# Performance work log

Hardware: AMD Instinct MI355X
Metric: run time of the kernel (lower is better)

Reference implementation:

```python
import jax, jax.numpy as jnp
import numpy as np

N = 100_000        # event nodes
E = 1_600_000      # directed edges (avg degree 16)
DIM = 256          # coordinate box size (input_dimension)
POOL = 4           # pool_size of all pooling layers


def gconv(nodes, feats, edges, W):
    """PointNet-style graph conv: msg = [f_src ; pos_src - pos_dst] @ W, max-aggregated at dst."""
    src, dst = edges[0], edges[1]
    msg = jnp.concatenate([feats[src], nodes[src] - nodes[dst]], axis=1) @ W  # [E, out]
    agg = jax.ops.segment_max(msg, dst, num_segments=nodes.shape[0])
    return jnp.where(jnp.isfinite(agg), agg, 0.0)  # nodes with no in-edges -> 0


def pool(nodes, feats, edges, pool_size, grid, self_loop):
    """Voxel-grid max pooling: cluster nodes into grid^3 cells, max-pool features,
    remap edges to cluster ids (duplicate edges are harmless under max aggregation)."""
    cell = jnp.clip(jnp.floor(nodes / pool_size).astype(jnp.int32), 0, grid - 1)
    cid = (cell[:, 0] * grid + cell[:, 1]) * grid + cell[:, 2]
    n_cells = grid ** 3
    nf = jax.ops.segment_max(feats, cid, num_segments=n_cells)
    nf = jnp.where(jnp.isfinite(nf), nf, 0.0)  # empty cells -> 0
    ii = jnp.arange(n_cells)
    nn = jnp.stack([ii // (grid * grid), (ii // grid) % grid, ii % grid], axis=1).astype(feats.dtype)
    ne = cid[edges]
    if self_loop:
        loops = jnp.tile(jnp.arange(n_cells, dtype=ne.dtype), (2, 1))
        ne = jnp.concatenate([ne, loops], axis=1)
    return nn, nf, ne


def forward(nodes, features, edges, W1, W2, W3, W4, W5, W6, W7, Wl, bl):
    relu = lambda x: jnp.maximum(x, 0.0)
    x = relu(gconv(nodes, features, edges, W1))              # [N, 8]
    x = relu(gconv(nodes, x, edges, W2))                     # [N, 16]
    nodes, x, edges = pool(nodes, x, edges, POOL, DIM // POOL, True)   # 64^3 cells
    x = relu(gconv(nodes, x, edges, W3))                     # [64^3, 32]
    x = relu(gconv(nodes, x, edges, W4))                     # [64^3, 32]
    nodes, x, edges = pool(nodes, x, edges, POOL, 64 // POOL, False)   # 16^3 cells
    x = relu(gconv(nodes, x, edges, W5))                     # [16^3, 64]
    x = relu(gconv(nodes, x, edges, W6))
    x = relu(gconv(nodes, x, edges, W7))
    # QuantGraphPoolOut: max-pool onto fixed 4x4x4 grid, flatten to [1, 4096]
    cell = jnp.clip(jnp.floor(nodes / POOL).astype(jnp.int32), 0, 3)
    cid = (cell[:, 0] * 4 + cell[:, 1]) * 4 + cell[:, 2]
    xo = jax.ops.segment_max(x, cid, num_segments=64)        # [64, 64]
    xo = jnp.where(jnp.isfinite(xo), xo, 0.0).reshape(1, -1)  # [1, 4096]
    # dropout is identity in eval mode
    return xo @ Wl + bl                                      # [1, 100]


def setup_inputs() -> dict:
    key = jax.random.key(0)
    ks = jax.random.split(key, 12)

    def w(k, i, o):  # conv weight: (input_dim + 3 pos dims, output_dim)
        return jax.random.normal(k, (i + 3, o), dtype=jnp.float32) * (1.0 / np.sqrt(i + 3))

    nodes = jax.random.uniform(ks[0], (N, 3), dtype=jnp.float32) * DIM
    features = jax.random.normal(ks[1], (N, 1), dtype=jnp.float32)
    edges = jax.random.randint(ks[2], (2, E), 0, N, dtype=jnp.int32)
    return {
        "nodes": nodes, "features": features, "edges": edges,
        "W1": w(ks[3], 1, 8), "W2": w(ks[4], 8, 16), "W3": w(ks[5], 16, 32),
        "W4": w(ks[6], 32, 32), "W5": w(ks[7], 32, 64), "W6": w(ks[8], 64, 64),
        "W7": w(ks[9], 64, 64),
        "Wl": jax.random.normal(ks[10], (4096, 100), dtype=jnp.float32) * (1.0 / 64.0),
        "bl": jnp.zeros((100,), dtype=jnp.float32),
    }


def reference(nodes, features, edges, W1, W2, W3, W4, W5, W6, W7, Wl, bl):
    return forward(nodes, features, edges, W1, W2, W3, W4, W5, W6, W7, Wl, bl)
```

## Files before the change

kernel.cpp:

```cpp
#include <hip/hip_runtime.h>

#define NN 100000
#define NE 1600000
#define C1 262144
#define C2 4096
#define BSH 7
#define BSZ 128
#define NB 782
#define PA_EDGES 8192
#define PA_IT (PA_EDGES / 256)
#define JMASK 0xFFFFF

__device__ __forceinline__ int parent2(int c) {
    return ((c >> 14) << 8) | (((c >> 8) & 15) << 4) | ((c >> 2) & 15);
}
__device__ __forceinline__ float4 max4(float4 a, float4 b) {
    return make_float4(fmaxf(a.x, b.x), fmaxf(a.y, b.y), fmaxf(a.z, b.z), fmaxf(a.w, b.w));
}
__device__ __forceinline__ float4 fma4(float s, float4 w, float4 acc) {
    return make_float4(s * w.x + acc.x, s * w.y + acc.y, s * w.z + acc.z, s * w.w + acc.w);
}

__global__ __launch_bounds__(256)
void cidhist_k(const float* __restrict__ nodes, int* __restrict__ cid,
               int* __restrict__ cntN) {
    int i = blockIdx.x * 256 + threadIdx.x;
    if (i >= NN) return;
    int cx = min(max((int)floorf(nodes[3 * i]     * 0.25f), 0), 63);
    int cy = min(max((int)floorf(nodes[3 * i + 1] * 0.25f), 0), 63);
    int cz = min(max((int)floorf(nodes[3 * i + 2] * 0.25f), 0), 63);
    int c = (cx * 64 + cy) * 64 + cz;
    cid[i] = c;
    atomicAdd(&cntN[c], 1);
}

__global__ __launch_bounds__(256)
void oclist_k(const int* __restrict__ cntN, int* __restrict__ oclist,
              int* __restrict__ jmap, int* __restrict__ ocount) {
    int c = blockIdx.x * 256 + threadIdx.x;
    bool occ = cntN[c] > 0;
    unsigned long long b = __ballot(occ);
    int lane = threadIdx.x & 63;
    int cnt = __popcll(b);
    int base = 0;
    if (cnt) {
        if (lane == 0) base = atomicAdd(ocount, cnt);
        base = __shfl(base, 0);
    }
    int pre = __popcll(b & ((1ull << lane) - 1));
    int j = occ ? base + pre : -1;
    jmap[c] = j;
    if (occ) oclist[j] = c;
}

__global__ __launch_bounds__(256)
void scan1_k(const int* __restrict__ cnt, int n, int* __restrict__ offs,
             int* __restrict__ bsum) {
    __shared__ int ws[4];
    int t = threadIdx.x, lane = t & 63, w = t >> 6;
    int base = blockIdx.x * 2048 + t * 8;
    int v[8]; int s = 0;
    #pragma unroll
    for (int i = 0; i < 8; ++i) { v[i] = (base + i < n) ? cnt[base + i] : 0; s += v[i]; }
    int sc = s;
    #pragma unroll
    for (int off = 1; off < 64; off <<= 1) { int o = __shfl_up(sc, off); if (lane >= off) sc += o; }
    if (lane == 63) ws[w] = sc;
    __syncthreads();
    int wbase = 0;
    for (int i = 0; i < w; ++i) wbase += ws[i];
    int run = wbase + sc - s;
    #pragma unroll
    for (int i = 0; i < 8; ++i) { if (base + i < n) offs[base + i] = run; run += v[i]; }
    if (t == 255) bsum[blockIdx.x] = wbase + sc;
}

__global__ __launch_bounds__(256)
void scan2_k(int* __restrict__ bsum, int nb) {
    __shared__ int ws[4];
    int t = threadIdx.x, lane = t & 63, w = t >> 6;
    int v = (t < nb) ? bsum[t] : 0;
    int sc = v;
    #pragma unroll
    for (int off = 1; off < 64; off <<= 1) { int o = __shfl_up(sc, off); if (lane >= off) sc += o; }
    if (lane == 63) ws[w] = sc;
    __syncthreads();
    int wbase = 0;
    for (int i = 0; i < w; ++i) wbase += ws[i];
    if (t < nb) bsum[t] = wbase + sc - v;
    if (t == 255) bsum[nb] = ws[0] + ws[1] + ws[2] + ws[3];
}

__global__ __launch_bounds__(256)
void scan3_k(int* __restrict__ offs, int n, const int* __restrict__ bsum, int nb) {
    int i = blockIdx.x * 256 + threadIdx.x;
    if (i < n) offs[i] += bsum[i >> 11];
    else if (i == n) offs[n] = bsum[nb];
}

__global__ __launch_bounds__(256)
void nscatter_k(const int* __restrict__ cid, const int* __restrict__ offsN,
                int* __restrict__ cntN, int* __restrict__ rank, int* __restrict__ nidx) {
    int i = blockIdx.x * 256 + threadIdx.x;
    if (i >= NN) return;
    int c = cid[i];
    int pos = offsN[c] + atomicAdd(&cntN[c], -1) - 1;
    rank[i] = pos;
    nidx[pos] = i;
}

__global__ __launch_bounds__(256)
void permute_k(const int* __restrict__ nidx, const float* __restrict__ nodes,
               const float* __restrict__ feats, const int* __restrict__ cid,
               const int* __restrict__ jmap,
               float* __restrict__ pnodes, float* __restrict__ pfeat,
               int* __restrict__ jsrcP) {
    int d = blockIdx.x * 256 + threadIdx.x;
    if (d >= NN) return;
    int i = nidx[d];
    pnodes[3 * d]     = nodes[3 * i];
    pnodes[3 * d + 1] = nodes[3 * i + 1];
    pnodes[3 * d + 2] = nodes[3 * i + 2];
    pfeat[d] = feats[i];
    int c = cid[i];
    unsigned packed = (unsigned)jmap[c] | ((unsigned)parent2(c) << 20);
    jsrcP[d] = (int)packed;
}

__global__ __launch_bounds__(256)
void bhist_k(const int* __restrict__ edst, const int* __restrict__ rank,
             int* __restrict__ btot) {
    __shared__ int h[NB];
    int tid = threadIdx.x;
    for (int i = tid; i < NB; i += 256) h[i] = 0;
    __syncthreads();
    int base = blockIdx.x * PA_EDGES;
    for (int i = 0; i < PA_IT; ++i) {
        int e = base + i * 256 + tid;
        if (e < NE) atomicAdd(&h[rank[edst[e]] >> BSH], 1);
    }
    __syncthreads();
    for (int i = tid; i < NB; i += 256) if (h[i]) atomicAdd(&btot[i], h[i]);
}

__global__ __launch_bounds__(256)
void scanB_k(const int* __restrict__ btot, int* __restrict__ bbase,
             int* __restrict__ cursor) {
    __shared__ int ws[4];
    int t = threadIdx.x, lane = t & 63, w = t >> 6;
    int i0 = 4 * t;
    int v[4]; int s = 0;
    #pragma unroll
    for (int q = 0; q < 4; ++q) { v[q] = (i0 + q < NB) ? btot[i0 + q] : 0; s += v[q]; }
    int sc = s;
    #pragma unroll
    for (int off = 1; off < 64; off <<= 1) { int o = __shfl_up(sc, off); if (lane >= off) sc += o; }
    if (lane == 63) ws[w] = sc;
    __syncthreads();
    int wb = 0;
    for (int q = 0; q < w; ++q) wb += ws[q];
    int run = wb + sc - s;
    #pragma unroll
    for (int q = 0; q < 4; ++q) {
        if (i0 + q <= NB) { bbase[i0 + q] = run; if (i0 + q < NB) cursor[i0 + q] = run; }
        run += v[q];
    }
}

__global__ __launch_bounds__(256)
void passA_k(const int* __restrict__ esrc, const int* __restrict__ edst,
             const int* __restrict__ rank, int* __restrict__ cursor,
             int2* __restrict__ ebuf) {
    __shared__ int hist[NB];
    __shared__ int lofs[NB + 1];
    __shared__ int gbase[NB];
    __shared__ int cnt2[NB];
    __shared__ int2 stage[PA_EDGES];
    __shared__ unsigned short sbid[PA_EDGES];
    __shared__ int ws[4];
    int tid = threadIdx.x, lane = tid & 63, w = tid >> 6;
    for (int i = tid; i < NB; i += 256) { hist[i] = 0; cnt2[i] = 0; }
    __syncthreads();
    int base = blockIdx.x * PA_EDGES;
    for (int i = 0; i < PA_IT; ++i) {
        int e = base + i * 256 + tid;
        if (e < NE) atomicAdd(&hist[rank[edst[e]] >> BSH], 1);
    }
    __syncthreads();
    int i0 = 4 * tid;
    int v[4]; int s = 0;
    #pragma unroll
    for (int q = 0; q < 4; ++q) { v[q] = (i0 + q < NB) ? hist[i0 + q] : 0; s += v[q]; }
    int sc = s;
    #pragma unroll
    for (int off = 1; off < 64; off <<= 1) { int o = __shfl_up(sc, off); if (lane >= off) sc += o; }
    if (lane == 63) ws[w] = sc;
    __syncthreads();
    int wb = 0;
    for (int q = 0; q < w; ++q) wb += ws[q];
    int run = wb + sc - s;
    #pragma unroll
    for (int q = 0; q < 4; ++q) {
        if (i0 + q <= NB) lofs[i0 + q] = run;
        run += v[q];
    }
    __syncthreads();
    for (int b = tid; b < NB; b += 256) {
        int c = hist[b];
        gbase[b] = c ? atomicAdd(&cursor[b], c) : 0;
    }
    __syncthreads();
    for (int i = 0; i < PA_IT; ++i) {
        int e = base + i * 256 + tid;
        if (e < NE) {
            int rd = rank[edst[e]], rs = rank[esrc[e]];
            int b = rd >> BSH;
            int p = lofs[b] + atomicAdd(&cnt2[b], 1);
            stage[p] = make_int2(rs, rd);
            sbid[p] = (unsigned short)b;
        }
    }
    __syncthreads();
    int nval = min(PA_EDGES, NE - base);
    for (int k = tid; k < nval; k += 256) {
        int b = sbid[k];
        ebuf[gbase[b] + (k - lofs[b])] = stage[k];
    }
}

__global__ __launch_bounds__(256)
void passB_k(const int2* __restrict__ ebuf, const int* __restrict__ bbase,
             const int* __restrict__ jsrcP,
             int* __restrict__ offs0, int* __restrict__ srcs0, int* __restrict__ csrc0) {
    __shared__ int cnt[BSZ];
    __shared__ int pos[BSZ];
    __shared__ int ws[4];
    int b = blockIdx.x, tid = threadIdx.x, lane = tid & 63, w = tid >> 6;
    int d0 = b << BSH;
    int range = min(BSZ, NN - d0);
    if (tid < BSZ) cnt[tid] = 0;
    __syncthreads();
    int r0 = bbase[b], r1 = bbase[b + 1];
    for (int k = r0 + tid; k < r1; k += 256) atomicAdd(&cnt[ebuf[k].y & (BSZ - 1)], 1);
    __syncthreads();
    int v = (tid < BSZ) ? cnt[tid] : 0;
    int sc = v;
    #pragma unroll
    for (int off = 1; off < 64; off <<= 1) { int o = __shfl_up(sc, off); if (lane >= off) sc += o; }
    if (lane == 63) ws[w] = sc;
    __syncthreads();
    int wb = 0;
    for (int q = 0; q < w; ++q) wb += ws[q];
    int rel = wb + sc - v;
    if (tid < range) offs0[d0 + tid] = r0 + rel;
    if (tid == 0) offs0[min(d0 + BSZ, NN)] = r1;
    if (tid < BSZ) pos[tid] = r0 + rel;
    __syncthreads();
    for (int k = r0 + tid; k < r1; k += 256) {
        int2 pr = ebuf[k];
        int di = pr.y & (BSZ - 1);
        int p = atomicAdd(&pos[di], 1);
        int rs = pr.x;
        srcs0[p] = rs;
        csrc0[p] = jsrcP[rs];
    }
}

__global__ __launch_bounds__(256)
void masklist_k(const int* __restrict__ offsN, const int* __restrict__ offs0,
                const int* __restrict__ csrc0,
                int* __restrict__ l2off, int* __restrict__ l2num,
                int* __restrict__ l2src, int* __restrict__ l2cursor) {
    __shared__ unsigned long long words[64];
    __shared__ int wpre[64];
    __shared__ int sbase;
    int d2 = blockIdx.x, tid = threadIdx.x;
    if (tid < 64) words[tid] = 0;
    __syncthreads();
    int x2 = d2 >> 8, y2 = (d2 >> 4) & 15, z2 = d2 & 15;
    int child = tid >> 2, sub = tid & 3;
    int i = child >> 4, jj = (child >> 2) & 3, k = child & 3;
    int d1 = ((x2 * 4 + i) * 64 + (y2 * 4 + jj)) * 64 + (z2 * 4 + k);
    int e0 = offs0[offsN[d1]], e1 = offs0[offsN[d1 + 1]];
    for (int t = e0 + sub; t < e1; t += 4) {
        int s2 = (int)(((unsigned)csrc0[t]) >> 20);
        atomicOr(&words[s2 >> 6], 1ull << (s2 & 63));
    }
    __syncthreads();
    if (tid < 64) {
        int pc = __popcll(words[tid]);
        int sc = pc;
        #pragma unroll
        for (int off = 1; off < 64; off <<= 1) {
            int o = __shfl_up(sc, off);
            if (tid >= off) sc += o;
        }
        wpre[tid] = sc - pc;
        if (tid == 63) {
            l2num[d2] = sc;
            int bb = atomicAdd(l2cursor, sc);
            l2off[d2] = bb;
            sbase = bb;
        }
    }
    __syncthreads();
    if (tid < 64) {
        unsigned long long wb = words[tid];
        int p = sbase + wpre[tid];
        while (wb) {
            int b = __builtin_ctzll(wb);
            wb &= wb - 1;
            l2src[p++] = (tid << 6) | b;
        }
    }
}

template<int CI, int CO>
__global__ __launch_bounds__(256)
void xform0_k(const float* __restrict__ pnodes, const float* __restrict__ f,
              const float* __restrict__ W, float* __restrict__ h) {
    __shared__ float sW[(CI + 3) * CO];
    for (int i = threadIdx.x; i < (CI + 3) * CO; i += 256) sW[i] = W[i];
    __syncthreads();
    int gid = blockIdx.x * 256 + threadIdx.x;
    int i = gid / CO, ch = gid - i * CO;
    if (i >= NN) return;
    float s = pnodes[3 * i] * sW[CI * CO + ch] + pnodes[3 * i + 1] * sW[(CI + 1) * CO + ch]
            + pnodes[3 * i + 2] * sW[(CI + 2) * CO + ch];
    #pragma unroll
    for (int k = 0; k < CI; ++k) s += f[(size_t)i * CI + k] * sW[k * CO + ch];
    h[(size_t)i * CO + ch] = s;
}

__global__ __launch_bounds__(256)
void gatherL0f_k(const float* __restrict__ pnodes, const float* __restrict__ h1,
                 const float* __restrict__ W1pos,
                 const float* __restrict__ W2,
                 const int* __restrict__ offs, const int* __restrict__ srcs,
                 float* __restrict__ h2) {
    __shared__ float sW1[24];
    __shared__ float sW2[176];
    __shared__ float f1s[32][8];
    int tid = threadIdx.x;
    if (tid < 24) sW1[tid] = W1pos[tid];
    if (tid < 176) sW2[tid] = W2[tid];
    __syncthreads();
    int gid = blockIdx.x * 256 + tid;
    int d = gid >> 3, ch = gid & 7;
    int dbase = blockIdx.x * 32;
    if (d < NN) {
        float c = pnodes[3 * d] * sW1[ch] + pnodes[3 * d + 1] * sW1[8 + ch] + pnodes[3 * d + 2] * sW1[16 + ch];
        float m0 = c, m1 = c, m2 = c, m3 = c;
        int e0 = offs[d], e1 = offs[d + 1];
        int t = e0;
        for (; t + 4 <= e1; t += 4) {
            int s0 = srcs[t], s1 = srcs[t + 1], s2 = srcs[t + 2], s3 = srcs[t + 3];
            m0 = fmaxf(m0, h1[(size_t)s0 * 8 + ch]);
            m1 = fmaxf(m1, h1[(size_t)s1 * 8 + ch]);
            m2 = fmaxf(m2, h1[(size_t)s2 * 8 + ch]);
            m3 = fmaxf(m3, h1[(size_t)s3 * 8 + ch]);
        }
        for (; t < e1; ++t) m0 = fmaxf(m0, h1[(size_t)srcs[t] * 8 + ch]);
        f1s[d - dbase][ch] = fmaxf(fmaxf(m0, m1), fmaxf(m2, m3)) - c;
    }
    __syncthreads();
    #pragma unroll
    for (int rep = 0; rep < 2; ++rep) {
        int dL = (tid >> 4) + rep * 16, ch2 = tid & 15;
        int dg = dbase + dL;
        if (dg < NN) {
            float s = pnodes[3 * dg] * sW2[128 + ch2] + pnodes[3 * dg + 1] * sW2[144 + ch2]
                    + pnodes[3 * dg + 2] * sW2[160 + ch2];
            #pragma unroll
            for (int k = 0; k < 8; ++k) s += f1s[dL][k] * sW2[k * 16 + ch2];
            h2[(size_t)dg * 16 + ch2] = s;
        }
    }
}

__global__ __launch_bounds__(256)
void gatherL0v4_k(const float* __restrict__ pnodes, const float* __restrict__ h,
                  const float* __restrict__ Wpos,
                  const int* __restrict__ offs, const int* __restrict__ srcs,
                  float* __restrict__ out) {
    __shared__ float sW[48];
    int tid = threadIdx.x;
    if (tid < 48) sW[tid] = Wpos[tid];
    __syncthreads();
    int gid = blockIdx.x * 256 + tid;
    int d = gid >> 2, q = gid & 3;
    if (d >= NN) return;
    float px = pnodes[3 * d], py = pnodes[3 * d + 1], pz = pnodes[3 * d + 2];
    float4 w0 = *(const float4*)&sW[q * 4];
    float4 w1 = *(const float4*)&sW[16 + q * 4];
    float4 w2 = *(const float4*)&sW[32 + q * 4];
    float4 c = make_float4(px * w0.x + py * w1.x + pz * w2.x, px * w0.y + py * w1.y + pz * w2.y,
                           px * w0.z + py * w1.z + pz * w2.z, px * w0.w + py * w1.w + pz * w2.w);
    float4 m0 = c, m1 = c, m2 = c, m3 = c;
    int e0 = offs[d], e1 = offs[d + 1];
    int t = e0;
    for (; t + 4 <= e1; t += 4) {
        int s0 = srcs[t], s1 = srcs[t + 1], s2 = srcs[t + 2], s3 = srcs[t + 3];
        m0 = max4(m0, *(const float4*)&h[(size_t)s0 * 16 + q * 4]);
        m1 = max4(m1, *(const float4*)&h[(size_t)s1 * 16 + q * 4]);
        m2 = max4(m2, *(const float4*)&h[(size_t)s2 * 16 + q * 4]);
        m3 = max4(m3, *(const float4*)&h[(size_t)s3 * 16 + q * 4]);
    }
    for (; t < e1; ++t) m0 = max4(m0, *(const float4*)&h[(size_t)srcs[t] * 16 + q * 4]);
    float4 m = max4(max4(m0, m1), max4(m2, m3));
    *(float4*)&out[(size_t)d * 16 + q * 4] = make_float4(m.x - c.x, m.y - c.y, m.z - c.z, m.w - c.w);
}

__global__ __launch_bounds__(256)
void pxformL1_k(const float* __restrict__ f2, const int* __restrict__ offsN,
                const int* __restrict__ oclist, const int* __restrict__ ocount,
                const float* __restrict__ W3, float* __restrict__ h) {
    __shared__ float sW[19 * 32];
    __shared__ float nf[8][16];
    for (int i = threadIdx.x; i < 19 * 32; i += 256) sW[i] = W3[i];
    int gid = blockIdx.x * 256 + threadIdx.x;
    int j = gid >> 5, ch = gid & 31;
    int lj = threadIdx.x >> 5;
    bool valid = j < *ocount;
    int d = valid ? oclist[j] : 0;
    if (valid && ch < 16) {
        float m = 0.f;
        int n0 = offsN[d], n1 = offsN[d + 1];
        for (int n = n0; n < n1; ++n) m = fmaxf(m, f2[(size_t)n * 16 + ch]);
        nf[lj][ch] = m;
    }
    __syncthreads();
    if (!valid) return;
    float px = (float)(d >> 12), py = (float)((d >> 6) & 63), pz = (float)(d & 63);
    float s = px * sW[16 * 32 + ch] + py * sW[17 * 32 + ch] + pz * sW[18 * 32 + ch];
    #pragma unroll
    for (int k = 0; k < 16; ++k) s += nf[lj][k] * sW[k * 32 + ch];
    h[(size_t)j * 32 + ch] = s;
}

__global__ __launch_bounds__(256)
void gatherL1f_k(const float* __restrict__ h, const float* __restrict__ W3pos,
                 const float* __restrict__ W4,
                 const int* __restrict__ offsN, const int* __restrict__ offs0,
                 const int* __restrict__ csrc0,
                 const int* __restrict__ oclist, const int* __restrict__ ocount,
                 float* __restrict__ hnext) {
    __shared__ float sWp[96];
    __shared__ float sW4[35 * 32];
    __shared__ float gsT[32][33];
    int tid = threadIdx.x;
    if (tid < 96) sWp[tid] = W3pos[tid];
    for (int i = tid; i < 35 * 32; i += 256) sW4[i] = W4[i];
    __syncthreads();
    int gid = blockIdx.x * 256 + tid;
    int j = gid >> 3, q = gid & 7;
    int lj = tid >> 3;
    bool valid = j < *ocount;
    int d = 0;
    float px = 0, py = 0, pz = 0;
    float4 c = make_float4(0, 0, 0, 0);
    if (valid) {
        d = oclist[j];
        px = (float)(d >> 12); py = (float)((d >> 6) & 63); pz = (float)(d & 63);
        float4 w0 = *(const float4*)&sWp[q * 4];
        float4 w1 = *(const float4*)&sWp[32 + q * 4];
        float4 w2 = *(const float4*)&sWp[64 + q * 4];
        c = make_float4(px * w0.x + py * w1.x + pz * w2.x, px * w0.y + py * w1.y + pz * w2.y,
                        px * w0.z + py * w1.z + pz * w2.z, px * w0.w + py * w1.w + pz * w2.w);
        float4 self = *(const float4*)&h[(size_t)j * 32 + q * 4];
        float4 m0 = max4(c, self), m1 = m0, m2 = m0, m3 = m0;
        int e0 = offs0[offsN[d]], e1 = offs0[offsN[d + 1]];
        int t = e0;
        for (; t + 4 <= e1; t += 4) {
            int s0 = csrc0[t] & JMASK, s1 = csrc0[t + 1] & JMASK;
            int s2 = csrc0[t + 2] & JMASK, s3 = csrc0[t + 3] & JMASK;
            m0 = max4(m0, *(const float4*)&h[(size_t)s0 * 32 + q * 4]);
            m1 = max4(m1, *(const float4*)&h[(size_t)s1 * 32 + q * 4]);
            m2 = max4(m2, *(const float4*)&h[(size_t)s2 * 32 + q * 4]);
            m3 = max4(m3, *(const float4*)&h[(size_t)s3 * 32 + q * 4]);
        }
        for (; t < e1; ++t) m0 = max4(m0, *(const float4*)&h[(size_t)(csrc0[t] & JMASK) * 32 + q * 4]);
        float4 m = max4(max4(m0, m1), max4(m2, m3));
        gsT[q * 4 + 0][lj] = m.x - c.x;
        gsT[q * 4 + 1][lj] = m.y - c.y;
        gsT[q * 4 + 2][lj] = m.z - c.z;
        gsT[q * 4 + 3][lj] = m.w - c.w;
    }
    __syncthreads();
    if (!valid) return;
    float4 s4;
    {
        float4 w0 = *(const float4*)&sW4[32 * 32 + q * 4];
        float4 w1 = *(const float4*)&sW4[33 * 32 + q * 4];
        float4 w2 = *(const float4*)&sW4[34 * 32 + q * 4];
        s4 = make_float4(px * w0.x + py * w1.x + pz * w2.x, px * w0.y + py * w1.y + pz * w2.y,
                         px * w0.z + py * w1.z + pz * w2.z, px * w0.w + py * w1.w + pz * w2.w);
    }
    #pragma unroll
    for (int k = 0; k < 32; ++k) {
        float g = gsT[k][lj];
        s4 = fma4(g, *(const float4*)&sW4[k * 32 + q * 4], s4);
    }
    *(float4*)&hnext[(size_t)j * 32 + q * 4] = s4;
}

__global__ __launch_bounds__(256)
void gatherL1_k(const float* __restrict__ h, const float* __restrict__ Wpos,
                const int* __restrict__ offsN, const int* __restrict__ offs0,
                const int* __restrict__ csrc0,
                const int* __restrict__ oclist, const int* __restrict__ ocount,
                float* __restrict__ g) {
    __shared__ float sW[96];
    int tid = threadIdx.x;
    if (tid < 96) sW[tid] = Wpos[tid];
    __syncthreads();
    int gid = blockIdx.x * 256 + tid;
    int j = gid >> 3, q = gid & 7;
    if (j >= *ocount) return;
    int d = oclist[j];
    float px = (float)(d >> 12), py = (float)((d >> 6) & 63), pz = (float)(d & 63);
    float4 w0 = *(const float4*)&sW[q * 4];
    float4 w1 = *(const float4*)&sW[32 + q * 4];
    float4 w2 = *(const float4*)&sW[64 + q * 4];
    float4 c = make_float4(px * w0.x + py * w1.x + pz * w2.x, px * w0.y + py * w1.y + pz * w2.y,
                           px * w0.z + py * w1.z + pz * w2.z, px * w0.w + py * w1.w + pz * w2.w);
    float4 self = *(const float4*)&h[(size_t)j * 32 + q * 4];
    float4 m0 = max4(c, self), m1 = m0, m2 = m0, m3 = m0;
    int e0 = offs0[offsN[d]], e1 = offs0[offsN[d + 1]];
    int t = e0;
    for (; t + 4 <= e1; t += 4) {
        int s0 = csrc0[t] & JMASK, s1 = csrc0[t + 1] & JMASK;
        int s2 = csrc0[t + 2] & JMASK, s3 = csrc0[t + 3] & JMASK;
        m0 = max4(m0, *(const float4*)&h[(size_t)s0 * 32 + q * 4]);
        m1 = max4(m1, *(const float4*)&h[(size_t)s1 * 32 + q * 4]);
        m2 = max4(m2, *(const float4*)&h[(size_t)s2 * 32 + q * 4]);
        m3 = max4(m3, *(const float4*)&h[(size_t)s3 * 32 + q * 4]);
    }
    for (; t < e1; ++t) m0 = max4(m0, *(const float4*)&h[(size_t)(csrc0[t] & JMASK) * 32 + q * 4]);
    float4 m = max4(max4(m0, m1), max4(m2, m3));
    *(float4*)&g[(size_t)j * 32 + q * 4] = make_float4(m.x - c.x, m.y - c.y, m.z - c.z, m.w - c.w);
}

__global__ __launch_bounds__(256)
void pool2x_k(const float* __restrict__ Gc, const int* __restrict__ jmap,
              const float* __restrict__ W5, float* __restrict__ h5) {
    __shared__ float part[8][32];
    __shared__ float nf2row[32];
    int d2 = blockIdx.x, tid = threadIdx.x;
    int x2 = d2 >> 8, y2 = (d2 >> 4) & 15, z2 = d2 & 15;
    int ch = tid & 31, grp = tid >> 5;
    float m = 0.f;
    #pragma unroll
    for (int cc = 0; cc < 8; ++cc) {
        int child = grp * 8 + cc;
        int i = child >> 4, jj = (child >> 2) & 3, k = child & 3;
        int d1 = ((x2 * 4 + i) * 64 + (y2 * 4 + jj)) * 64 + (z2 * 4 + k);
        int cj = jmap[d1];
        if (cj >= 0) m = fmaxf(m, Gc[(size_t)cj * 32 + ch]);
    }
    part[grp][ch] = m;
    __syncthreads();
    if (tid < 32) {
        float mm = part[0][tid];
        #pragma unroll
        for (int g = 1; g < 8; ++g) mm = fmaxf(mm, part[g][tid]);
        nf2row[tid] = mm;
    }
    __syncthreads();
    if (tid < 64) {
        float s = x2 * W5[32 * 64 + tid] + y2 * W5[33 * 64 + tid] + z2 * W5[34 * 64 + tid];
        #pragma unroll
        for (int k = 0; k < 32; ++k) s += nf2row[k] * W5[k * 64 + tid];
        h5[(size_t)d2 * 64 + tid] = s;
    }
}

template<bool FUSE, bool WRITE_G>
__global__ __launch_bounds__(256)
void gconvL2_k(const float* __restrict__ h, const float* __restrict__ Wpos,
               const int* __restrict__ l2off, const int* __restrict__ l2num,
               const int* __restrict__ l2src,
               const float* __restrict__ Wn,
               float* __restrict__ gout, float* __restrict__ hnext) {
    __shared__ float red[16][64];
    __shared__ float grow[64];
    int d2 = blockIdx.x, tid = threadIdx.x;
    int x2 = d2 >> 8, y2 = (d2 >> 4) & 15, z2 = d2 & 15;
    int q = tid & 15, grp = tid >> 4;
    int n0 = l2off[d2], num = l2num[d2];
    int per = (num + 15) >> 4;
    int s = n0 + grp * per;
    int e = min(n0 + num, s + per);
    float4 m0 = make_float4(-1e30f, -1e30f, -1e30f, -1e30f);
    float4 m1 = m0, m2 = m0, m3 = m0;
    int t = s;
    for (; t + 4 <= e; t += 4) {
        int s0 = l2src[t], s1 = l2src[t + 1], s2 = l2src[t + 2], s3 = l2src[t + 3];
        m0 = max4(m0, *(const float4*)&h[(size_t)s0 * 64 + q * 4]);
        m1 = max4(m1, *(const float4*)&h[(size_t)s1 * 64 + q * 4]);
        m2 = max4(m2, *(const float4*)&h[(size_t)s2 * 64 + q * 4]);
        m3 = max4(m3, *(const float4*)&h[(size_t)s3 * 64 + q * 4]);
    }
    for (; t < e; ++t) m0 = max4(m0, *(const float4*)&h[(size_t)l2src[t] * 64 + q * 4]);
    float4 m = max4(max4(m0, m1), max4(m2, m3));
    red[grp][q * 4 + 0] = m.x;
    red[grp][q * 4 + 1] = m.y;
    red[grp][q * 4 + 2] = m.z;
    red[grp][q * 4 + 3] = m.w;
    __syncthreads();
    if (tid < 64) {
        int ch = tid;
        float mm = red[0][ch];
        #pragma unroll
        for (int g = 1; g < 16; ++g) mm = fmaxf(mm, red[g][ch]);
        float c = x2 * Wpos[ch] + y2 * Wpos[64 + ch] + z2 * Wpos[128 + ch];
        mm = fmaxf(mm, fmaxf(c, h[(size_t)d2 * 64 + ch]));
        float g = mm - c;
        if (WRITE_G) gout[(size_t)d2 * 64 + ch] = g;
        if (FUSE) grow[ch] = g;
    }
    if (FUSE) {
        __syncthreads();
        if (tid < 64) {
            float s2v = x2 * Wn[64 * 64 + tid] + y2 * Wn[65 * 64 + tid] + z2 * Wn[66 * 64 + tid];
            #pragma unroll
            for (int k = 0; k < 64; ++k) s2v += grow[k] * Wn[k * 64 + tid];
            hnext[(size_t)d2 * 64 + tid] = s2v;
        }
    }
}

__global__ __launch_bounds__(256)
void outpool_k(const float* __restrict__ g7, float* __restrict__ xo) {
    int gid = blockIdx.x * 256 + threadIdx.x;
    if (gid >= 64 * 64) return;
    int oc = gid >> 6, ch = gid & 63;
    int cx = oc >> 4, cy = (oc >> 2) & 3, cz = oc & 3;
    float m = 0.f;
    for (int tc = 0; tc < 64; ++tc) {
        int i = tc >> 4, j = (tc >> 2) & 3, k = tc & 3;
        int d2 = ((cx * 4 + i) * 16 + (cy * 4 + j)) * 16 + (cz * 4 + k);
        m = fmaxf(m, g7[(size_t)d2 * 64 + ch]);
    }
    xo[(size_t)oc * 64 + ch] = m;
}

__global__ __launch_bounds__(64)
void linear_k(const float* __restrict__ xo, const float* __restrict__ Wl,
              const float* __restrict__ bl, float* __restrict__ out) {
    int j = blockIdx.x;
    float s = 0.f;
    for (int i = threadIdx.x; i < 4096; i += 64) s += xo[i] * Wl[(size_t)i * 100 + j];
    #pragma unroll
    for (int off = 32; off; off >>= 1) s += __shfl_down(s, off);
    if (threadIdx.x == 0) out[j] = s + bl[j];
}

extern "C" void kernel_launch(void* const* d_in, const int* in_sizes, int n_in,
                              void* d_out, int out_size, void* d_ws, size_t ws_size,
                              hipStream_t stream) {
    (void)in_sizes; (void)n_in; (void)out_size;
    const float* nodes = (const float*)d_in[0];
    const float* feats = (const float*)d_in[1];
    const int*   edges = (const int*)d_in[2];
    const int*   esrc  = edges;
    const int*   edst  = edges + NE;
    const float* W1 = (const float*)d_in[3];
    const float* W2 = (const float*)d_in[4];
    const float* W3 = (const float*)d_in[5];
    const float* W4 = (const float*)d_in[6];
    const float* W5 = (const float*)d_in[7];
    const float* W6 = (const float*)d_in[8];
    const float* W7 = (const float*)d_in[9];
    const float* Wl = (const float*)d_in[10];
    const float* bl = (const float*)d_in[11];
    float* out = (float*)d_out;

    char* ws = (char*)d_ws;
    size_t off = 0;
    auto alloc = [&](size_t bytes) { void* p = ws + off; off = (off + bytes + 255) & ~(size_t)255; return p; };
    int*   cntN    = (int*)alloc((size_t)C1 * 4);
    int*   ocount  = (int*)alloc(4);
    int*   btot    = (int*)alloc((size_t)NB * 4);
    int*   l2cursor= (int*)alloc(4);
    size_t zero_bytes = off;
    int*   bsum   = (int*)alloc(260 * 4);
    int*   bbase  = (int*)alloc((size_t)(NB + 1) * 4);
    int*   cursor = (int*)alloc((size_t)NB * 4);
    int*   cid    = (int*)alloc((size_t)NN * 4);
    int*   rank   = (int*)alloc((size_t)NN * 4);
    int*   nidx   = (int*)alloc((size_t)NN * 4);
    int*   offsN  = (int*)alloc((size_t)(C1 + 1) * 4);
    int*   offs0  = (int*)alloc((size_t)(NN + 1) * 4);
    int*   srcs0  = (int*)alloc((size_t)NE * 4);
    int*   csrc0  = (int*)alloc((size_t)NE * 4);
    int2*  ebuf   = (int2*)alloc((size_t)NE * 8);
    int*   oclist = (int*)alloc((size_t)NN * 4);
    int*   jmap   = (int*)alloc((size_t)C1 * 4);
    int*   jsrcP  = (int*)alloc((size_t)NN * 4);
    int*   l2off  = (int*)alloc((size_t)C2 * 4);
    int*   l2num  = (int*)alloc((size_t)C2 * 4);
    int*   l2srcA = (int*)alloc((size_t)NE * 4);
    float* pnodes = (float*)alloc((size_t)NN * 3 * 4);
    float* pfeat  = (float*)alloc((size_t)NN * 4);
    float* A      = (float*)alloc((size_t)NN * 48 * 4);
    float* Hc     = (float*)alloc((size_t)NN * 32 * 4);
    float* Gc     = (float*)alloc((size_t)NN * 32 * 4);
    float* h5     = (float*)alloc((size_t)C2 * 64 * 4);
    float* h6     = (float*)alloc((size_t)C2 * 64 * 4);
    float* h7     = (float*)alloc((size_t)C2 * 64 * 4);
    float* g7     = (float*)alloc((size_t)C2 * 64 * 4);
    float* xo     = (float*)alloc((size_t)64 * 64 * 4);
    if (ws_size < off) return;

    float* h1 = A;
    float* h2 = A + (size_t)NN * 16;
    float* f2 = A + (size_t)NN * 32;

    hipMemsetAsync(cntN, 0, zero_bytes, stream);

    auto gr = [](long long n) { return (int)((n + 255) / 256); };
    const int nbC1 = (C1 + 2047) / 2048;
    const int gPA  = (NE + PA_EDGES - 1) / PA_EDGES;

    cidhist_k<<<gr(NN), 256, 0, stream>>>(nodes, cid, cntN);
    oclist_k<<<C1 / 256, 256, 0, stream>>>(cntN, oclist, jmap, ocount);
    scan1_k<<<nbC1, 256, 0, stream>>>(cntN, C1, offsN, bsum);
    scan2_k<<<1, 256, 0, stream>>>(bsum, nbC1);
    scan3_k<<<gr(C1 + 1), 256, 0, stream>>>(offsN, C1, bsum, nbC1);
    nscatter_k<<<gr(NN), 256, 0, stream>>>(cid, offsN, cntN, rank, nidx);
    permute_k<<<gr(NN), 256, 0, stream>>>(nidx, nodes, feats, cid, jmap, pnodes, pfeat, jsrcP);
    bhist_k<<<gPA, 256, 0, stream>>>(edst, rank, btot);
    scanB_k<<<1, 256, 0, stream>>>(btot, bbase, cursor);
    passA_k<<<gPA, 256, 0, stream>>>(esrc, edst, rank, cursor, ebuf);
    passB_k<<<NB, 256, 0, stream>>>(ebuf, bbase, jsrcP, offs0, srcs0, csrc0);
    masklist_k<<<C2, 256, 0, stream>>>(offsN, offs0, csrc0, l2off, l2num, l2srcA, l2cursor);

    xform0_k<1, 8><<<gr((long long)NN * 8), 256, 0, stream>>>(pnodes, pfeat, W1, h1);
    gatherL0f_k<<<gr((long long)NN * 8), 256, 0, stream>>>(pnodes, h1, W1 + 1 * 8, W2, offs0, srcs0, h2);
    gatherL0v4_k<<<gr((long long)NN * 4), 256, 0, stream>>>(pnodes, h2, W2 + 8 * 16, offs0, srcs0, f2);

    pxformL1_k<<<gr((long long)NN * 32), 256, 0, stream>>>(f2, offsN, oclist, ocount, W3, Hc);
    gatherL1f_k<<<gr((long long)NN * 8), 256, 0, stream>>>(Hc, W3 + 16 * 32, W4, offsN, offs0, csrc0, oclist, ocount, Gc);
    gatherL1_k<<<gr((long long)NN * 8), 256, 0, stream>>>(Gc, W4 + 32 * 32, offsN, offs0, csrc0, oclist, ocount, Hc);

    pool2x_k<<<C2, 256, 0, stream>>>(Hc, jmap, W5, h5);
    gconvL2_k<true,  false><<<C2, 256, 0, stream>>>(h5, W5 + 32 * 64, l2off, l2num, l2srcA, W6, nullptr, h6);
    gconvL2_k<true,  false><<<C2, 256, 0, stream>>>(h6, W6 + 64 * 64, l2off, l2num, l2srcA, W7, nullptr, h7);
    gconvL2_k<false, true ><<<C2, 256, 0, stream>>>(h7, W7 + 64 * 64, l2off, l2num, l2srcA, nullptr, g7, nullptr);

    outpool_k<<<16, 256, 0, stream>>>(g7, xo);
    linear_k<<<100, 64, 0, stream>>>(xo, Wl, bl, out);
}
```

Before: 465.2 us.

## Reindex level-1 cells in hierarchical Morton-like order grouped by parent cell

Level-1 cell ids become a key built from the parent 16^3 cell and the 4x4x4 child offset, so the 64 children of each parent are contiguous. The node sort, the occupied-cell list and the CSR offsets follow this order, which lets masklist read one contiguous edge range per parent and lets pool2x index jmap directly. Gathers in later layers should also get better locality, because neighbouring cells now sit close together in memory. Coordinates are decoded from the key with a helper, which adds a few integer operations per use.

```diff
diff --git a/kernel.cpp b/kernel.cpp
--- a/kernel.cpp
+++ b/kernel.cpp
@@ -11,8 +11,11 @@
 #define PA_IT (PA_EDGES / 256)
 #define JMASK 0xFFFFF
 
-__device__ __forceinline__ int parent2(int c) {
-    return ((c >> 14) << 8) | (((c >> 8) & 15) << 4) | ((c >> 2) & 15);
+__device__ __forceinline__ void key2xyz(int key, float& x, float& y, float& z) {
+    int d2 = key >> 6, ch = key & 63;
+    x = (float)((((d2 >> 8) & 15) << 2) | (ch >> 4));
+    y = (float)((((d2 >> 4) & 15) << 2) | ((ch >> 2) & 3));
+    z = (float)(((d2 & 15) << 2) | (ch & 3));
 }
 __device__ __forceinline__ float4 max4(float4 a, float4 b) {
     return make_float4(fmaxf(a.x, b.x), fmaxf(a.y, b.y), fmaxf(a.z, b.z), fmaxf(a.w, b.w));
@@ -29,9 +32,11 @@
     int cx = min(max((int)floorf(nodes[3 * i]     * 0.25f), 0), 63);
     int cy = min(max((int)floorf(nodes[3 * i + 1] * 0.25f), 0), 63);
     int cz = min(max((int)floorf(nodes[3 * i + 2] * 0.25f), 0), 63);
-    int c = (cx * 64 + cy) * 64 + cz;
-    cid[i] = c;
-    atomicAdd(&cntN[c], 1);
+    int d2 = ((cx >> 2) * 16 + (cy >> 2)) * 16 + (cz >> 2);
+    int ch = ((cx & 3) * 4 + (cy & 3)) * 4 + (cz & 3);
+    int key = (d2 << 6) | ch;
+    cid[i] = key;
+    atomicAdd(&cntN[key], 1);
 }
 
 __global__ __launch_bounds__(256)
@@ -123,7 +128,7 @@
     pnodes[3 * d + 2] = nodes[3 * i + 2];
     pfeat[d] = feats[i];
     int c = cid[i];
-    unsigned packed = (unsigned)jmap[c] | ((unsigned)parent2(c) << 20);
+    unsigned packed = (unsigned)jmap[c] | (((unsigned)c >> 6) << 20);
     jsrcP[d] = (int)packed;
 }
 
@@ -277,12 +282,9 @@
     int d2 = blockIdx.x, tid = threadIdx.x;
     if (tid < 64) words[tid] = 0;
     __syncthreads();
-    int x2 = d2 >> 8, y2 = (d2 >> 4) & 15, z2 = d2 & 15;
-    int child = tid >> 2, sub = tid & 3;
-    int i = child >> 4, jj = (child >> 2) & 3, k = child & 3;
-    int d1 = ((x2 * 4 + i) * 64 + (y2 * 4 + jj)) * 64 + (z2 * 4 + k);
-    int e0 = offs0[offsN[d1]], e1 = offs0[offsN[d1 + 1]];
-    for (int t = e0 + sub; t < e1; t += 4) {
+    int e0 = offs0[offsN[d2 << 6]];
+    int e1 = offs0[offsN[(d2 + 1) << 6]];
+    for (int t = e0 + tid; t < e1; t += 256) {
         int s2 = (int)(((unsigned)csrc0[t]) >> 20);
         atomicOr(&words[s2 >> 6], 1ull << (s2 & 63));
     }
@@ -431,7 +433,8 @@
     }
     __syncthreads();
     if (!valid) return;
-    float px = (float)(d >> 12), py = (float)((d >> 6) & 63), pz = (float)(d & 63);
+    float px, py, pz;
+    key2xyz(d, px, py, pz);
     float s = px * sW[16 * 32 + ch] + py * sW[17 * 32 + ch] + pz * sW[18 * 32 + ch];
     #pragma unroll
     for (int k = 0; k < 16; ++k) s += nf[lj][k] * sW[k * 32 + ch];
@@ -456,17 +459,15 @@
     int j = gid >> 3, q = gid & 7;
     int lj = tid >> 3;
     bool valid = j < *ocount;
-    int d = 0;
     float px = 0, py = 0, pz = 0;
-    float4 c = make_float4(0, 0, 0, 0);
     if (valid) {
-        d = oclist[j];
-        px = (float)(d >> 12); py = (float)((d >> 6) & 63); pz = (float)(d & 63);
+        int d = oclist[j];
+        key2xyz(d, px, py, pz);
         float4 w0 = *(const float4*)&sWp[q * 4];
         float4 w1 = *(const float4*)&sWp[32 + q * 4];
         float4 w2 = *(const float4*)&sWp[64 + q * 4];
-        c = make_float4(px * w0.x + py * w1.x + pz * w2.x, px * w0.y + py * w1.y + pz * w2.y,
-                        px * w0.z + py * w1.z + pz * w2.z, px * w0.w + py * w1.w + pz * w2.w);
+        float4 c = make_float4(px * w0.x + py * w1.x + pz * w2.x, px * w0.y + py * w1.y + pz * w2.y,
+                               px * w0.z + py * w1.z + pz * w2.z, px * w0.w + py * w1.w + pz * w2.w);
         float4 self = *(const float4*)&h[(size_t)j * 32 + q * 4];
         float4 m0 = max4(c, self), m1 = m0, m2 = m0, m3 = m0;
         int e0 = offs0[offsN[d]], e1 = offs0[offsN[d + 1]];
@@ -518,7 +519,8 @@
     int j = gid >> 3, q = gid & 7;
     if (j >= *ocount) return;
     int d = oclist[j];
-    float px = (float)(d >> 12), py = (float)((d >> 6) & 63), pz = (float)(d & 63);
+    float px, py, pz;
+    key2xyz(d, px, py, pz);
     float4 w0 = *(const float4*)&sW[q * 4];
     float4 w1 = *(const float4*)&sW[32 + q * 4];
     float4 w2 = *(const float4*)&sW[64 + q * 4];
@@ -552,10 +554,7 @@
     float m = 0.f;
     #pragma unroll
     for (int cc = 0; cc < 8; ++cc) {
-        int child = grp * 8 + cc;
-        int i = child >> 4, jj = (child >> 2) & 3, k = child & 3;
-        int d1 = ((x2 * 4 + i) * 64 + (y2 * 4 + jj)) * 64 + (z2 * 4 + k);
-        int cj = jmap[d1];
+        int cj = jmap[(d2 << 6) | (grp * 8 + cc)];
         if (cj >= 0) m = fmaxf(m, Gc[(size_t)cj * 32 + ch]);
     }
     part[grp][ch] = m;
```

Measured after the change: 462.8 us. About the same (-0.5%).
